# Kernel optimization log

Measured on AMD Instinct MI355X. Metric: run time of the kernel, lower is better.

The kernel has to match this reference:

```python
import jax, jax.numpy as jnp
import numpy as np

B, L, D, H = 2, 2048, 1024, 16
HD = D // H  # 64
SCALE = 1.0 / np.sqrt(HD)


def _rope(x, cos, sin):
    # x: (B,H,L,HD); cos/sin: (B,H,L,HD//2). Half-split RoPE as in the torch code.
    d = x.shape[-1] // 2
    x1, x2 = x[..., :d], x[..., d:]
    return jnp.concatenate([x1 * cos - x2 * sin, x1 * sin + x2 * cos], axis=-1)


def setup_inputs() -> dict:
    key = jax.random.key(0)
    ks = jax.random.split(key, 5)
    x = jax.random.normal(ks[0], (B, L, D), dtype=jnp.float32)
    rope_cos = jax.random.uniform(ks[1], (B, L, D // 2), dtype=jnp.float32)
    rope_sin = jax.random.uniform(ks[2], (B, L, D // 2), dtype=jnp.float32)
    # scale weights ~ 1/sqrt(fan_in) so attention logits stay well-conditioned
    W_qkv = jax.random.normal(ks[3], (D, 3 * D), dtype=jnp.float32) / np.sqrt(D)
    W_o = jax.random.normal(ks[4], (D, D), dtype=jnp.float32) / np.sqrt(D)
    mask = jnp.ones((B, L), dtype=jnp.int32)
    return {"x": x, "rope_cos": rope_cos, "rope_sin": rope_sin,
            "W_qkv": W_qkv, "W_o": W_o, "mask": mask}


def reference(x, rope_cos, rope_sin, W_qkv, W_o, mask):
    b, l, d = x.shape
    # fused QKV projection (no bias)
    qkv = (x @ W_qkv).reshape(b, l, 3, H, HD)
    q, k, v = (jnp.transpose(qkv[:, :, i], (0, 2, 1, 3)) for i in range(3))  # (B,H,L,HD)
    cos = jnp.transpose(rope_cos.reshape(b, l, H, HD // 2), (0, 2, 1, 3))
    sin = jnp.transpose(rope_sin.reshape(b, l, H, HD // 2), (0, 2, 1, 3))
    q = _rope(q, cos, sin)
    k = _rope(k, cos, sin)
    scores = jnp.einsum("bhqd,bhkd->bhqk", q, k) * SCALE  # (B,H,L,L)
    scores = jnp.where(mask[:, None, None, :] == 0, -jnp.inf, scores)
    attn = jax.nn.softmax(scores, axis=-1)
    out = jnp.einsum("bhqk,bhkd->bhqd", attn, v)  # (B,H,L,HD)
    out = jnp.transpose(out, (0, 2, 1, 3)).reshape(b, l, d)
    return out @ W_o
```

## Files before the change

### kernel.cpp

```cpp
#include <hip/hip_runtime.h>

typedef unsigned short u16;
typedef unsigned int u32;
typedef __attribute__((ext_vector_type(8))) short bf16x8;
typedef __attribute__((ext_vector_type(4))) float f32x4;

#define MFMA_BF16(a, b, c) __builtin_amdgcn_mfma_f32_16x16x32_bf16(a, b, c, 0, 0, 0)

__device__ __forceinline__ u16 f2bf(float f) {
    union { float f; u32 i; } v; v.f = f;
    u32 r = v.i + 0x7fffu + ((v.i >> 16) & 1u);
    return (u16)(r >> 16);
}
__device__ __forceinline__ u32 pack2bf(float a, float b) {
    u32 ua = __float_as_uint(a) + 0x8000u;
    u32 ub = __float_as_uint(b) + 0x8000u;
    return __builtin_amdgcn_perm(ub, ua, 0x07060302u);
}
__device__ __forceinline__ void load_lds16(const void* g, void* l) {
    __builtin_amdgcn_global_load_lds(
        (const __attribute__((address_space(1))) void*)g,
        (__attribute__((address_space(3))) void*)l,
        16, 0, 0);
}

__global__ __launch_bounds__(256) void prep(
    const float* __restrict__ x, const float* __restrict__ wqkv,
    const float* __restrict__ wo, const int* __restrict__ mask,
    u16* __restrict__ xb, u16* __restrict__ wqkv_t, u16* __restrict__ wo_t,
    float* __restrict__ bias2) {
    __shared__ u16 tile[64][66];
    int bid = blockIdx.x;
    if (bid < 1024) {
        const float* in; u16* out; int N, r;
        if (bid < 768) { in = wqkv; out = wqkv_t; N = 3072; r = bid; }
        else           { in = wo;   out = wo_t;   N = 1024; r = bid - 768; }
        int k0 = (r & 15) * 64, n0 = (r >> 4) * 64;
        int tx = threadIdx.x & 63, ty0 = threadIdx.x >> 6;
        #pragma unroll
        for (int i = 0; i < 16; i++) {
            int ty = ty0 + i * 4;
            tile[ty][tx] = f2bf(in[(size_t)(k0 + ty) * N + n0 + tx]);
        }
        __syncthreads();
        #pragma unroll
        for (int i = 0; i < 16; i++) {
            int ty = ty0 + i * 4;
            out[(size_t)(n0 + ty) * 1024 + k0 + tx] = tile[tx][ty];
        }
    } else if (bid < 5120) {
        int i = (bid - 1024) * 1024 + threadIdx.x * 4;
        float4 v = *(const float4*)(x + i);
        uint2 o;
        o.x = pack2bf(v.x, v.y);
        o.y = pack2bf(v.z, v.w);
        *(uint2*)(xb + i) = o;
    } else {
        int i = (bid - 5120) * 256 + threadIdx.x;
        bias2[i] = mask[i] ? -28.8539008f : -1e30f;
    }
}

__global__ __launch_bounds__(256) void gemm_qkv_rope(
    const u16* __restrict__ xb, const u16* __restrict__ wt,
    const float* __restrict__ cosb, const float* __restrict__ sinb,
    u16* __restrict__ Qo, u16* __restrict__ Ko, u16* __restrict__ Vt) {
    __shared__ __align__(16) u16 sA[128 * 32];
    __shared__ __align__(16) u16 sB[128 * 32];
    const int lane = threadIdx.x & 63, wv = threadIdx.x >> 6;
    const int l16 = lane & 15, quad = lane >> 4;
    const int wr = wv >> 1, wc = wv & 1;
    const int m0 = blockIdx.x * 128;
    const int nw = blockIdx.y * 128 + wc * 64;
    const int sec = nw >> 10;
    const int h   = (nw >> 6) & 15;

    const int sr = lane >> 2, sc = (lane & 3) * 8;
    const u16* gA0 = xb + (size_t)(m0 + wv * 32 + sr) * 1024 + sc;
    const u16* gA1 = gA0 + 16 * 1024;
    const u16* gB0 = wt + (size_t)(blockIdx.y * 128 + wv * 32 + sr) * 1024 + sc;
    const u16* gB1 = gB0 + 16 * 1024;
    u16* lA0 = &sA[wv * 1024]; u16* lA1 = lA0 + 512;
    u16* lB0 = &sB[wv * 1024]; u16* lB1 = lB0 + 512;

    f32x4 acc[4][4];
    #pragma unroll
    for (int i = 0; i < 4; i++)
        #pragma unroll
        for (int j = 0; j < 4; j++) acc[i][j] = {0.f, 0.f, 0.f, 0.f};

    for (int k0 = 0; k0 < 1024; k0 += 32) {
        load_lds16(gA0 + k0, lA0);
        load_lds16(gA1 + k0, lA1);
        load_lds16(gB0 + k0, lB0);
        load_lds16(gB1 + k0, lB1);
        __syncthreads();

        bf16x8 af[4], bf[4];
        #pragma unroll
        for (int i = 0; i < 4; i++)
            af[i] = *(const bf16x8*)&sA[(wr * 64 + i * 16 + l16) * 32 + quad * 8];
        #pragma unroll
        for (int j = 0; j < 4; j++)
            bf[j] = *(const bf16x8*)&sB[(wc * 64 + j * 16 + l16) * 32 + quad * 8];
        #pragma unroll
        for (int i = 0; i < 4; i++)
            #pragma unroll
            for (int j = 0; j < 4; j++)
                acc[i][j] = MFMA_BF16(af[i], bf[j], acc[i][j]);
        __syncthreads();
    }

    #pragma unroll
    for (int i = 0; i < 4; i++) {
        #pragma unroll
        for (int r = 0; r < 4; r++) {
            int m = m0 + wr * 64 + i * 16 + quad * 4 + r;
            int b = m >> 11, l = m & 2047;
            int bh = b * 16 + h;
            if (sec == 2) {
                Vt[((bh * 64 +  0 + l16) * 2048) + l] = f2bf(acc[i][0][r]);
                Vt[((bh * 64 + 16 + l16) * 2048) + l] = f2bf(acc[i][1][r]);
                Vt[((bh * 64 + 32 + l16) * 2048) + l] = f2bf(acc[i][2][r]);
                Vt[((bh * 64 + 48 + l16) * 2048) + l] = f2bf(acc[i][3][r]);
            } else {
                const float* cs = cosb + (size_t)m * 512 + h * 32;
                const float* sn = sinb + (size_t)m * 512 + h * 32;
                float c0 = cs[l16],      s0 = sn[l16];
                float c1 = cs[16 + l16], s1 = sn[16 + l16];
                float x1a = acc[i][0][r], x2a = acc[i][2][r];
                float x1b = acc[i][1][r], x2b = acc[i][3][r];
                u16* dst = (sec == 0 ? Qo : Ko) + ((size_t)bh * 2048 + l) * 64;
                dst[l16]      = f2bf(x1a * c0 - x2a * s0);
                dst[16 + l16] = f2bf(x1b * c1 - x2b * s1);
                dst[32 + l16] = f2bf(x1a * s0 + x2a * c0);
                dst[48 + l16] = f2bf(x1b * s1 + x2b * c1);
            }
        }
    }
}

__global__ __launch_bounds__(512, 4) void attn_kernel(
    const u16* __restrict__ Q, const u16* __restrict__ K,
    const u16* __restrict__ Vt, const float* __restrict__ bias2,
    u16* __restrict__ AO) {
    __shared__ __align__(16) char raw[40960];
    u16* sK = (u16*)raw;
    u16* sV = sK + 4096;
    const int lane = threadIdx.x & 63, wv = threadIdx.x >> 6;
    const int l16 = lane & 15, quad = lane >> 4;
    const int qs = wv & 3, ks = wv >> 2;
    const int bh = blockIdx.x >> 4;
    const int qt = blockIdx.x & 15;
    const int q0 = qt * 128 + qs * 32;
    const int b = bh >> 4, h = bh & 15;
    const float SCALE2 = 0.18033688f;

    const u16* qbase = Q + ((size_t)bh * 2048 + q0) * 64;
    bf16x8 q0lo = *(const bf16x8*)(qbase + l16 * 64 + quad * 8);
    bf16x8 q0hi = *(const bf16x8*)(qbase + l16 * 64 + 32 + quad * 8);
    bf16x8 q1lo = *(const bf16x8*)(qbase + (16 + l16) * 64 + quad * 8);
    bf16x8 q1hi = *(const bf16x8*)(qbase + (16 + l16) * 64 + 32 + quad * 8);

    union { u32 w[4]; bf16x8 v; } ones;
    ones.w[0] = ones.w[1] = ones.w[2] = ones.w[3] = 0x3F803F80u;

    f32x4 O[2][4], Ol[2];
    #pragma unroll
    for (int t = 0; t < 2; t++) {
        #pragma unroll
        for (int j = 0; j < 4; j++) O[t][j] = {0.f, 0.f, 0.f, 0.f};
        Ol[t] = {0.f, 0.f, 0.f, 0.f};
    }

    const int krow_l = qs * 8 + (lane >> 3);
    const int kcol_s = (lane & 7) ^ ((krow_l & 3) | (((krow_l >> 3) & 1) << 2));
    const u16* gKs = K + (size_t)bh * 2048 * 64 + (ks * 1024 + krow_l) * 64 + kcol_s * 8;
    u16* sKw = sK + ks * 2048 + qs * 512;
    const int vrow_l = qs * 16 + (lane >> 2);
    const int vcol_s = (lane & 3) ^ ((vrow_l >> 1) & 3);
    const u16* gVs = Vt + (size_t)bh * 64 * 2048 + vrow_l * 2048 + ks * 1024 + vcol_s * 8;
    u16* sVw = sV + ks * 2048 + qs * 512;

    const int r0 = (l16 >> 2) * 8 + (l16 & 3);
    const int kk0 = (l16 & 3) | (((l16 >> 2) & 1) << 2);
    const int sA0 = quad ^ kk0;
    const int kOff0 = ks * 2048 + r0 * 64 + sA0 * 8;
    const int kOff1 = ks * 2048 + r0 * 64 + (sA0 ^ 4) * 8;
    const int vOff = ks * 2048 + l16 * 32 + (quad ^ ((l16 >> 1) & 3)) * 8;

    const float* bbase = bias2 + b * 2048 + ks * 1024 + quad * 8;

    for (int key0 = 0; key0 < 1024; key0 += 32) {
        load_lds16(gKs + key0 * 64, sKw);
        load_lds16(gVs + key0, sVw);
        __syncthreads();

        bf16x8 ka0 = *(const bf16x8*)&sK[kOff0];
        bf16x8 ka1 = *(const bf16x8*)&sK[kOff1];
        bf16x8 kb0 = *(const bf16x8*)&sK[kOff0 + 256];
        bf16x8 kb1 = *(const bf16x8*)&sK[kOff1 + 256];
        bf16x8 v0 = *(const bf16x8*)&sV[vOff];
        bf16x8 v1 = *(const bf16x8*)&sV[vOff + 512];
        bf16x8 v2 = *(const bf16x8*)&sV[vOff + 1024];
        bf16x8 v3 = *(const bf16x8*)&sV[vOff + 1536];
        float4 bi0 = *(const float4*)(bbase + key0);
        float4 bi1 = *(const float4*)(bbase + key0 + 4);

        f32x4 S00 = {0.f,0.f,0.f,0.f}, S01 = S00, S10 = S00, S11 = S00;
        S00 = MFMA_BF16(ka0, q0lo, S00); S00 = MFMA_BF16(ka1, q0hi, S00);
        S01 = MFMA_BF16(ka0, q1lo, S01); S01 = MFMA_BF16(ka1, q1hi, S01);
        S10 = MFMA_BF16(kb0, q0lo, S10); S10 = MFMA_BF16(kb1, q0hi, S10);
        S11 = MFMA_BF16(kb0, q1lo, S11); S11 = MFMA_BF16(kb1, q1hi, S11);

        union { u32 w[4]; bf16x8 v; } pb0, pb1;
        float a0 = __builtin_amdgcn_exp2f(fmaf(S00[0], SCALE2, bi0.x));
        float a1 = __builtin_amdgcn_exp2f(fmaf(S00[1], SCALE2, bi0.y));
        float a2 = __builtin_amdgcn_exp2f(fmaf(S00[2], SCALE2, bi0.z));
        float a3 = __builtin_amdgcn_exp2f(fmaf(S00[3], SCALE2, bi0.w));
        float a4 = __builtin_amdgcn_exp2f(fmaf(S10[0], SCALE2, bi1.x));
        float a5 = __builtin_amdgcn_exp2f(fmaf(S10[1], SCALE2, bi1.y));
        float a6 = __builtin_amdgcn_exp2f(fmaf(S10[2], SCALE2, bi1.z));
        float a7 = __builtin_amdgcn_exp2f(fmaf(S10[3], SCALE2, bi1.w));
        pb0.w[0] = pack2bf(a0, a1); pb0.w[1] = pack2bf(a2, a3);
        pb0.w[2] = pack2bf(a4, a5); pb0.w[3] = pack2bf(a6, a7);

        float c0 = __builtin_amdgcn_exp2f(fmaf(S01[0], SCALE2, bi0.x));
        float c1 = __builtin_amdgcn_exp2f(fmaf(S01[1], SCALE2, bi0.y));
        float c2 = __builtin_amdgcn_exp2f(fmaf(S01[2], SCALE2, bi0.z));
        float c3 = __builtin_amdgcn_exp2f(fmaf(S01[3], SCALE2, bi0.w));
        float c4 = __builtin_amdgcn_exp2f(fmaf(S11[0], SCALE2, bi1.x));
        float c5 = __builtin_amdgcn_exp2f(fmaf(S11[1], SCALE2, bi1.y));
        float c6 = __builtin_amdgcn_exp2f(fmaf(S11[2], SCALE2, bi1.z));
        float c7 = __builtin_amdgcn_exp2f(fmaf(S11[3], SCALE2, bi1.w));
        pb1.w[0] = pack2bf(c0, c1); pb1.w[1] = pack2bf(c2, c3);
        pb1.w[2] = pack2bf(c4, c5); pb1.w[3] = pack2bf(c6, c7);

        O[0][0] = MFMA_BF16(v0, pb0.v, O[0][0]);
        O[0][1] = MFMA_BF16(v1, pb0.v, O[0][1]);
        O[0][2] = MFMA_BF16(v2, pb0.v, O[0][2]);
        O[0][3] = MFMA_BF16(v3, pb0.v, O[0][3]);
        Ol[0]   = MFMA_BF16(ones.v, pb0.v, Ol[0]);
        O[1][0] = MFMA_BF16(v0, pb1.v, O[1][0]);
        O[1][1] = MFMA_BF16(v1, pb1.v, O[1][1]);
        O[1][2] = MFMA_BF16(v2, pb1.v, O[1][2]);
        O[1][3] = MFMA_BF16(v3, pb1.v, O[1][3]);
        Ol[1]   = MFMA_BF16(ones.v, pb1.v, Ol[1]);
        __syncthreads();
    }

    __syncthreads();
    f32x4* mb = (f32x4*)raw;
    if (ks == 1) {
        f32x4* base = mb + qs * 640 + lane;
        #pragma unroll
        for (int t = 0; t < 2; t++)
            #pragma unroll
            for (int j = 0; j < 4; j++)
                base[(t * 4 + j) * 64] = O[t][j];
        base[8 * 64] = Ol[0];
        base[9 * 64] = Ol[1];
    }
    __syncthreads();
    if (ks == 0) {
        f32x4* base = mb + qs * 640 + lane;
        #pragma unroll
        for (int t = 0; t < 2; t++)
            #pragma unroll
            for (int j = 0; j < 4; j++)
                O[t][j] += base[(t * 4 + j) * 64];
        Ol[0] += base[8 * 64];
        Ol[1] += base[9 * 64];
        #pragma unroll
        for (int t = 0; t < 2; t++) {
            float l = Ol[t][0];
            float inv = l > 0.f ? 1.0f / l : 0.f;
            #pragma unroll
            for (int j = 0; j < 4; j++) {
                uint2 o;
                o.x = pack2bf(O[t][j][0] * inv, O[t][j][1] * inv);
                o.y = pack2bf(O[t][j][2] * inv, O[t][j][3] * inv);
                u16* dst = AO + ((size_t)(b * 2048 + q0 + t * 16 + l16)) * 1024
                              + h * 64 + j * 16 + quad * 4;
                *(uint2*)dst = o;
            }
        }
    }
}

__global__ __launch_bounds__(256) void gemm_out(
    const u16* __restrict__ A, const u16* __restrict__ bt,
    float* __restrict__ out) {
    __shared__ __align__(16) u16 sA[128 * 32];
    __shared__ __align__(16) u16 sB[128 * 32];
    const int lane = threadIdx.x & 63, wv = threadIdx.x >> 6;
    const int l16 = lane & 15, quad = lane >> 4;
    const int wr = wv >> 1, wc = wv & 1;
    const int m0 = blockIdx.x * 128;
    const int n0 = blockIdx.y * 128;

    const int sr = lane >> 2, sc = (lane & 3) * 8;
    const u16* gA0 = A  + (size_t)(m0 + wv * 32 + sr) * 1024 + sc;
    const u16* gA1 = gA0 + 16 * 1024;
    const u16* gB0 = bt + (size_t)(n0 + wv * 32 + sr) * 1024 + sc;
    const u16* gB1 = gB0 + 16 * 1024;
    u16* lA0 = &sA[wv * 1024]; u16* lA1 = lA0 + 512;
    u16* lB0 = &sB[wv * 1024]; u16* lB1 = lB0 + 512;

    f32x4 acc[4][4];
    #pragma unroll
    for (int i = 0; i < 4; i++)
        #pragma unroll
        for (int j = 0; j < 4; j++) acc[i][j] = {0.f, 0.f, 0.f, 0.f};

    for (int k0 = 0; k0 < 1024; k0 += 32) {
        load_lds16(gA0 + k0, lA0);
        load_lds16(gA1 + k0, lA1);
        load_lds16(gB0 + k0, lB0);
        load_lds16(gB1 + k0, lB1);
        __syncthreads();

        bf16x8 af[4], bf[4];
        #pragma unroll
        for (int i = 0; i < 4; i++)
            af[i] = *(const bf16x8*)&sA[(wr * 64 + i * 16 + l16) * 32 + quad * 8];
        #pragma unroll
        for (int j = 0; j < 4; j++)
            bf[j] = *(const bf16x8*)&sB[(wc * 64 + j * 16 + l16) * 32 + quad * 8];
        #pragma unroll
        for (int i = 0; i < 4; i++)
            #pragma unroll
            for (int j = 0; j < 4; j++)
                acc[i][j] = MFMA_BF16(af[i], bf[j], acc[i][j]);
        __syncthreads();
    }

    #pragma unroll
    for (int i = 0; i < 4; i++) {
        #pragma unroll
        for (int r = 0; r < 4; r++) {
            int m = m0 + wr * 64 + i * 16 + quad * 4 + r;
            float* dst = out + (size_t)m * 1024 + n0 + wc * 64;
            dst[l16]      = acc[i][0][r];
            dst[16 + l16] = acc[i][1][r];
            dst[32 + l16] = acc[i][2][r];
            dst[48 + l16] = acc[i][3][r];
        }
    }
}

extern "C" void kernel_launch(void* const* d_in, const int* in_sizes, int n_in,
                              void* d_out, int out_size, void* d_ws, size_t ws_size,
                              hipStream_t stream) {
    const float* x    = (const float*)d_in[0];
    const float* cosb = (const float*)d_in[1];
    const float* sinb = (const float*)d_in[2];
    const float* wqkv = (const float*)d_in[3];
    const float* wo   = (const float*)d_in[4];
    const int*   mask = (const int*)d_in[5];
    float* out = (float*)d_out;

    u16* ws      = (u16*)d_ws;
    u16* wqkv_t  = ws;
    u16* wo_t    = wqkv_t + 3072 * 1024;
    u16* xb      = wo_t   + 1024 * 1024;
    u16* Qb      = xb     + 4096 * 1024;
    u16* Kb      = Qb     + 32 * 2048 * 64;
    u16* Vtb     = Kb     + 32 * 2048 * 64;
    u16* AO      = Vtb    + 32 * 2048 * 64;
    float* bias2 = (float*)(AO + 4096 * 1024);

    prep<<<5136, 256, 0, stream>>>(x, wqkv, wo, mask, xb, wqkv_t, wo_t, bias2);
    gemm_qkv_rope<<<dim3(32, 24), 256, 0, stream>>>(xb, wqkv_t, cosb, sinb, Qb, Kb, Vtb);
    attn_kernel<<<512, 512, 0, stream>>>(Qb, Kb, Vtb, bias2, AO);
    gemm_out<<<dim3(32, 8), 256, 0, stream>>>(AO, wo_t, out);
}
```

Baseline: 230.5 us.

## Deepen GEMM K-tile with XOR-swizzled LDS, stage V transpose, pack cos/sin

Both GEMMs now load a 64-wide K slice per iteration into XOR-swizzled shared memory, which halves the barrier count and avoids bank conflicts on the MFMA fragment reads. The V output of the QKV GEMM is transposed through LDS so it can be written to Vt as coalesced 16-byte stores instead of scattered 2-byte stores. Cos and sin are pre-packed into interleaved bf16 pairs in the prep kernel, stored in the AO workspace before attention uses it, so the RoPE epilogue does one 8-byte load per row. In exchange the QKV kernel uses more shared memory, and rounding cos/sin to bf16 adds some precision loss.

After: 217.0 us. 1.06x faster.

```diff
diff --git a/kernel.cpp b/kernel.cpp
--- a/kernel.cpp
+++ b/kernel.cpp
@@ -25,10 +25,11 @@
 }
 
 __global__ __launch_bounds__(256) void prep(
-    const float* __restrict__ x, const float* __restrict__ wqkv,
+    const float* __restrict__ x, const float* __restrict__ cosb,
+    const float* __restrict__ sinb, const float* __restrict__ wqkv,
     const float* __restrict__ wo, const int* __restrict__ mask,
     u16* __restrict__ xb, u16* __restrict__ wqkv_t, u16* __restrict__ wo_t,
-    float* __restrict__ bias2) {
+    u32* __restrict__ csp, float* __restrict__ bias2) {
     __shared__ u16 tile[64][66];
     int bid = blockIdx.x;
     if (bid < 1024) {
@@ -55,33 +56,43 @@
         o.x = pack2bf(v.x, v.y);
         o.y = pack2bf(v.z, v.w);
         *(uint2*)(xb + i) = o;
+    } else if (bid < 9216) {
+        int tid = (bid - 5120) * 256 + threadIdx.x;
+        int m = tid >> 8, h = (tid >> 4) & 15, d = tid & 15;
+        const float* cb = cosb + (size_t)m * 512 + h * 32 + d;
+        const float* sb = sinb + (size_t)m * 512 + h * 32 + d;
+        uint2 o;
+        o.x = pack2bf(cb[0], sb[0]);
+        o.y = pack2bf(cb[16], sb[16]);
+        *(uint2*)(csp + (size_t)m * 512 + h * 32 + 2 * d) = o;
     } else {
-        int i = (bid - 5120) * 256 + threadIdx.x;
+        int i = (bid - 9216) * 256 + threadIdx.x;
         bias2[i] = mask[i] ? -28.8539008f : -1e30f;
     }
 }
 
 __global__ __launch_bounds__(256) void gemm_qkv_rope(
     const u16* __restrict__ xb, const u16* __restrict__ wt,
-    const float* __restrict__ cosb, const float* __restrict__ sinb,
+    const u32* __restrict__ csp,
     u16* __restrict__ Qo, u16* __restrict__ Ko, u16* __restrict__ Vt) {
-    __shared__ __align__(16) u16 sA[128 * 32];
-    __shared__ __align__(16) u16 sB[128 * 32];
+    __shared__ __align__(16) char raw[34816];
+    u16* sA = (u16*)raw;
+    u16* sB = (u16*)(raw + 16384);
     const int lane = threadIdx.x & 63, wv = threadIdx.x >> 6;
     const int l16 = lane & 15, quad = lane >> 4;
     const int wr = wv >> 1, wc = wv & 1;
     const int m0 = blockIdx.x * 128;
-    const int nw = blockIdx.y * 128 + wc * 64;
+    const int y = blockIdx.y;
+    const int nw = y * 128 + wc * 64;
     const int sec = nw >> 10;
-    const int h   = (nw >> 6) & 15;
-
-    const int sr = lane >> 2, sc = (lane & 3) * 8;
-    const u16* gA0 = xb + (size_t)(m0 + wv * 32 + sr) * 1024 + sc;
-    const u16* gA1 = gA0 + 16 * 1024;
-    const u16* gB0 = wt + (size_t)(blockIdx.y * 128 + wv * 32 + sr) * 1024 + sc;
-    const u16* gB1 = gB0 + 16 * 1024;
-    u16* lA0 = &sA[wv * 1024]; u16* lA1 = lA0 + 512;
-    u16* lB0 = &sB[wv * 1024]; u16* lB1 = lB0 + 512;
+    const int h = (nw >> 6) & 15;
+
+    const int srow = lane >> 3, sp = lane & 7;
+    const int sc = (sp ^ srow) * 8;
+    const u16* gA = xb + (size_t)(m0 + wv * 32 + srow) * 1024 + sc;
+    const u16* gB = wt + (size_t)(y * 128 + wv * 32 + srow) * 1024 + sc;
+    u16* lA = sA + wv * 2048;
+    u16* lB = sB + wv * 2048;
 
     f32x4 acc[4][4];
     #pragma unroll
@@ -89,45 +100,71 @@
         #pragma unroll
         for (int j = 0; j < 4; j++) acc[i][j] = {0.f, 0.f, 0.f, 0.f};
 
-    for (int k0 = 0; k0 < 1024; k0 += 32) {
-        load_lds16(gA0 + k0, lA0);
-        load_lds16(gA1 + k0, lA1);
-        load_lds16(gB0 + k0, lB0);
-        load_lds16(gB1 + k0, lB1);
-        __syncthreads();
-
-        bf16x8 af[4], bf[4];
+    const int so = l16 & 7;
+    const int rdA = (wr * 64 + l16) * 64;
+    const int rdB = (wc * 64 + l16) * 64;
+
+    for (int k0 = 0; k0 < 1024; k0 += 64) {
+        #pragma unroll
+        for (int t = 0; t < 4; t++) {
+            load_lds16(gA + t * 8192 + k0, lA + t * 512);
+            load_lds16(gB + t * 8192 + k0, lB + t * 512);
+        }
+        __syncthreads();
+        #pragma unroll
+        for (int kk = 0; kk < 2; kk++) {
+            const int po = ((kk * 4 + quad) ^ so) * 8;
+            bf16x8 af[4], bf[4];
+            #pragma unroll
+            for (int i = 0; i < 4; i++)
+                af[i] = *(const bf16x8*)&sA[rdA + i * 1024 + po];
+            #pragma unroll
+            for (int j = 0; j < 4; j++)
+                bf[j] = *(const bf16x8*)&sB[rdB + j * 1024 + po];
+            #pragma unroll
+            for (int i = 0; i < 4; i++)
+                #pragma unroll
+                for (int j = 0; j < 4; j++)
+                    acc[i][j] = MFMA_BF16(af[i], bf[j], acc[i][j]);
+        }
+        __syncthreads();
+    }
+
+    const int b = m0 >> 11;
+    if (sec == 2) {
+        u32* vb = (u32*)raw;
+        const int l0 = m0 & 2047;
         #pragma unroll
         for (int i = 0; i < 4; i++)
-            af[i] = *(const bf16x8*)&sA[(wr * 64 + i * 16 + l16) * 32 + quad * 8];
-        #pragma unroll
-        for (int j = 0; j < 4; j++)
-            bf[j] = *(const bf16x8*)&sB[(wc * 64 + j * 16 + l16) * 32 + quad * 8];
-        #pragma unroll
-        for (int i = 0; i < 4; i++)
             #pragma unroll
             for (int j = 0; j < 4; j++)
-                acc[i][j] = MFMA_BF16(af[i], bf[j], acc[i][j]);
-        __syncthreads();
-    }
-
-    #pragma unroll
-    for (int i = 0; i < 4; i++) {
-        #pragma unroll
-        for (int r = 0; r < 4; r++) {
-            int m = m0 + wr * 64 + i * 16 + quad * 4 + r;
-            int b = m >> 11, l = m & 2047;
-            int bh = b * 16 + h;
-            if (sec == 2) {
-                Vt[((bh * 64 +  0 + l16) * 2048) + l] = f2bf(acc[i][0][r]);
-                Vt[((bh * 64 + 16 + l16) * 2048) + l] = f2bf(acc[i][1][r]);
-                Vt[((bh * 64 + 32 + l16) * 2048) + l] = f2bf(acc[i][2][r]);
-                Vt[((bh * 64 + 48 + l16) * 2048) + l] = f2bf(acc[i][3][r]);
-            } else {
-                const float* cs = cosb + (size_t)m * 512 + h * 32;
-                const float* sn = sinb + (size_t)m * 512 + h * 32;
-                float c0 = cs[l16],      s0 = sn[l16];
-                float c1 = cs[16 + l16], s1 = sn[16 + l16];
+                #pragma unroll
+                for (int rp = 0; rp < 2; rp++)
+                    vb[wc * 4352 + (j * 16 + l16) * 68 + wr * 32 + i * 8 + quad * 2 + rp]
+                        = pack2bf(acc[i][j][2 * rp], acc[i][j][2 * rp + 1]);
+        __syncthreads();
+        #pragma unroll
+        for (int t = 0; t < 8; t++) {
+            int R = wv * 32 + t * 4 + (lane >> 4);
+            int hh = R >> 6, d = R & 63;
+            uint4 v = *(uint4*)&vb[hh * 4352 + d * 68 + (lane & 15) * 4];
+            u16* dst = Vt + ((size_t)((b * 16 + ((y * 2 + hh) & 15)) * 64 + d)) * 2048
+                          + l0 + (lane & 15) * 8;
+            *(uint4*)dst = v;
+        }
+    } else {
+        #pragma unroll
+        for (int i = 0; i < 4; i++) {
+            #pragma unroll
+            for (int r = 0; r < 4; r++) {
+                int m = m0 + wr * 64 + i * 16 + quad * 4 + r;
+                int l = m & 2047;
+                int bh = b * 16 + h;
+                uint2 w = *(const uint2*)(csp + (size_t)m * 512 + h * 32 + 2 * l16);
+                float c0 = __uint_as_float(w.x << 16);
+                float s0 = __uint_as_float(w.x & 0xffff0000u);
+                float c1 = __uint_as_float(w.y << 16);
+                float s1 = __uint_as_float(w.y & 0xffff0000u);
                 float x1a = acc[i][0][r], x2a = acc[i][2][r];
                 float x1b = acc[i][1][r], x2b = acc[i][3][r];
                 u16* dst = (sec == 0 ? Qo : Ko) + ((size_t)bh * 2048 + l) * 64;
@@ -291,21 +328,20 @@
 __global__ __launch_bounds__(256) void gemm_out(
     const u16* __restrict__ A, const u16* __restrict__ bt,
     float* __restrict__ out) {
-    __shared__ __align__(16) u16 sA[128 * 32];
-    __shared__ __align__(16) u16 sB[128 * 32];
+    __shared__ __align__(16) u16 sA[128 * 64];
+    __shared__ __align__(16) u16 sB[128 * 64];
     const int lane = threadIdx.x & 63, wv = threadIdx.x >> 6;
     const int l16 = lane & 15, quad = lane >> 4;
     const int wr = wv >> 1, wc = wv & 1;
     const int m0 = blockIdx.x * 128;
     const int n0 = blockIdx.y * 128;
 
-    const int sr = lane >> 2, sc = (lane & 3) * 8;
-    const u16* gA0 = A  + (size_t)(m0 + wv * 32 + sr) * 1024 + sc;
-    const u16* gA1 = gA0 + 16 * 1024;
-    const u16* gB0 = bt + (size_t)(n0 + wv * 32 + sr) * 1024 + sc;
-    const u16* gB1 = gB0 + 16 * 1024;
-    u16* lA0 = &sA[wv * 1024]; u16* lA1 = lA0 + 512;
-    u16* lB0 = &sB[wv * 1024]; u16* lB1 = lB0 + 512;
+    const int srow = lane >> 3, sp = lane & 7;
+    const int sc = (sp ^ srow) * 8;
+    const u16* gA = A  + (size_t)(m0 + wv * 32 + srow) * 1024 + sc;
+    const u16* gB = bt + (size_t)(n0 + wv * 32 + srow) * 1024 + sc;
+    u16* lA = sA + wv * 2048;
+    u16* lB = sB + wv * 2048;
 
     f32x4 acc[4][4];
     #pragma unroll
@@ -313,25 +349,33 @@
         #pragma unroll
         for (int j = 0; j < 4; j++) acc[i][j] = {0.f, 0.f, 0.f, 0.f};
 
-    for (int k0 = 0; k0 < 1024; k0 += 32) {
-        load_lds16(gA0 + k0, lA0);
-        load_lds16(gA1 + k0, lA1);
-        load_lds16(gB0 + k0, lB0);
-        load_lds16(gB1 + k0, lB1);
-        __syncthreads();
-
-        bf16x8 af[4], bf[4];
-        #pragma unroll
-        for (int i = 0; i < 4; i++)
-            af[i] = *(const bf16x8*)&sA[(wr * 64 + i * 16 + l16) * 32 + quad * 8];
-        #pragma unroll
-        for (int j = 0; j < 4; j++)
-            bf[j] = *(const bf16x8*)&sB[(wc * 64 + j * 16 + l16) * 32 + quad * 8];
-        #pragma unroll
-        for (int i = 0; i < 4; i++)
+    const int so = l16 & 7;
+    const int rdA = (wr * 64 + l16) * 64;
+    const int rdB = (wc * 64 + l16) * 64;
+
+    for (int k0 = 0; k0 < 1024; k0 += 64) {
+        #pragma unroll
+        for (int t = 0; t < 4; t++) {
+            load_lds16(gA + t * 8192 + k0, lA + t * 512);
+            load_lds16(gB + t * 8192 + k0, lB + t * 512);
+        }
+        __syncthreads();
+        #pragma unroll
+        for (int kk = 0; kk < 2; kk++) {
+            const int po = ((kk * 4 + quad) ^ so) * 8;
+            bf16x8 af[4], bf[4];
+            #pragma unroll
+            for (int i = 0; i < 4; i++)
+                af[i] = *(const bf16x8*)&sA[rdA + i * 1024 + po];
             #pragma unroll
             for (int j = 0; j < 4; j++)
-                acc[i][j] = MFMA_BF16(af[i], bf[j], acc[i][j]);
+                bf[j] = *(const bf16x8*)&sB[rdB + j * 1024 + po];
+            #pragma unroll
+            for (int i = 0; i < 4; i++)
+                #pragma unroll
+                for (int j = 0; j < 4; j++)
+                    acc[i][j] = MFMA_BF16(af[i], bf[j], acc[i][j]);
+        }
         __syncthreads();
     }
 
@@ -369,9 +413,11 @@
     u16* Vtb     = Kb     + 32 * 2048 * 64;
     u16* AO      = Vtb    + 32 * 2048 * 64;
     float* bias2 = (float*)(AO + 4096 * 1024);
-
-    prep<<<5136, 256, 0, stream>>>(x, wqkv, wo, mask, xb, wqkv_t, wo_t, bias2);
-    gemm_qkv_rope<<<dim3(32, 24), 256, 0, stream>>>(xb, wqkv_t, cosb, sinb, Qb, Kb, Vtb);
+    u32* csp     = (u32*)AO;
+
+    prep<<<9232, 256, 0, stream>>>(x, cosb, sinb, wqkv, wo, mask,
+                                   xb, wqkv_t, wo_t, csp, bias2);
+    gemm_qkv_rope<<<dim3(32, 24), 256, 0, stream>>>(xb, wqkv_t, csp, Qb, Kb, Vtb);
     attn_kernel<<<512, 512, 0, stream>>>(Qb, Kb, Vtb, bias2, AO);
     gemm_out<<<dim3(32, 8), 256, 0, stream>>>(AO, wo_t, out);
 }
```
